# Kernel optimization log

Hardware: AMD Instinct MI355X
Metric: run time of the kernel (lower is better)

## Reference

```python
import jax, jax.numpy as jnp
import numpy as np

B, D, L, H = 4, 1024, 2048, 8
HD = D // H


def setup_inputs() -> dict:
    key = jax.random.key(0)
    k1, k2, k3, k4 = jax.random.split(key, 4)
    query = jax.random.normal(k1, (B, D, L), dtype=jnp.float32)
    mask = jax.random.randint(k2, (B, L), 0, 2, dtype=jnp.int32)
    W1 = jax.random.normal(k3, (2 * D, D), dtype=jnp.float32) * (D ** -0.5)
    Wq = jax.random.normal(k4, (D, D), dtype=jnp.float32) * (D ** -0.5)
    return {"query": query, "mask": mask, "W1": W1, "Wq": Wq}


def _split_heads(x):
    # [B, L, C] -> [B, H, L, C//H]
    b, l, c = x.shape
    return x.reshape(b, l, H, c // H).transpose(0, 2, 1, 3)


def reference(query, mask, W1, Wq):
    # 1x1 conv == channel GEMM; produce [B, L, out]
    temp = jnp.einsum('od,bdl->blo', W1, query)   # [B, L, 2D] (K|V)
    q = jnp.einsum('od,bdl->blo', Wq, query)      # [B, L, D]
    k, v = jnp.split(temp, 2, axis=-1)
    q = _split_heads(q) * (HD ** -0.5)            # [B, H, L, HD]
    k = _split_heads(k)
    v = _split_heads(v)
    scores = jnp.einsum('bhqd,bhkd->bhqk', q, k)  # [B, H, L, L]
    m = mask.astype(jnp.float32)[:, None, None, :]
    logits = scores + (-1e30) * (1.0 - m)
    weights = jax.nn.softmax(logits, axis=-1)     # dropout p=0 (eval)
    out = jnp.einsum('bhqk,bhkd->bhqd', weights, v)
    out = out.transpose(0, 2, 1, 3).reshape(B, L, D)  # merge heads
    return out.transpose(0, 2, 1)                 # [B, D, L]
```

## Files before the change

kernel.cpp:

```cpp
#include <hip/hip_runtime.h>
#include <hip/hip_bf16.h>

#define B_  4
#define D_  1024
#define L_  2048
#define H_  8
#define HD_ 128

typedef __attribute__((ext_vector_type(8))) short bf16x8;
typedef __attribute__((ext_vector_type(4))) float f32x4;

static __device__ __forceinline__ ushort f2bf(float f) {
    unsigned u = __float_as_uint(f);
    unsigned r = (u + 0x7fffu + ((u >> 16) & 1u)) >> 16;
    return (ushort)r;
}

static __device__ __forceinline__ unsigned cvt_pk_bf16(float lo, float hi) {
    unsigned r;
    asm("v_cvt_pk_bf16_f32 %0, %1, %2" : "=v"(r) : "v"(lo), "v"(hi));
    return r;
}

static __device__ __forceinline__ float exp2_fast(float x) {
#if __has_builtin(__builtin_amdgcn_exp2f)
    return __builtin_amdgcn_exp2f(x);
#else
    return exp2f(x);
#endif
}

static __device__ __forceinline__ void dma16(const ushort* g, ushort* l) {
    __builtin_amdgcn_global_load_lds(
        (const __attribute__((address_space(1))) void*)g,
        (__attribute__((address_space(3))) void*)l, 16, 0, 0);
}

__global__ void k_zero_out(float* __restrict__ out, int n) {
    int i = blockIdx.x * 256 + threadIdx.x;
    if (i < n) out[i] = 0.f;
}

__global__ void k_prep(const float* __restrict__ q, const float* __restrict__ W1,
                       const float* __restrict__ Wq, const int* __restrict__ mask,
                       ushort* __restrict__ Wb, ushort* __restrict__ Xt,
                       int* __restrict__ cidx, int* __restrict__ cnt) {
    __shared__ float tile[32][33];
    const int bid = blockIdx.x, t = threadIdx.x;
    if (bid < 8192) {
        int bx = bid & 63, by = (bid >> 6) & 31, bz = bid >> 11;
        int tx = t & 31, ty = t >> 5;
        int d0 = by * 32, l0 = bx * 32;
        const float* src = q + (size_t)bz * D_ * L_;
        for (int i = 0; i < 4; i++)
            tile[ty + 8 * i][tx] = src[(size_t)(d0 + ty + 8 * i) * L_ + l0 + tx];
        __syncthreads();
        ushort* dst = Xt + (size_t)bz * L_ * D_;
        for (int i = 0; i < 4; i++)
            dst[(size_t)(l0 + ty + 8 * i) * D_ + d0 + tx] = f2bf(tile[tx][ty + 8 * i]);
    } else if (bid < 8192 + 3072) {
        int i = (bid - 8192) * 256 + t;
        const int n1 = 2 * D_ * D_ / 4;
        float4 v = (i < n1) ? ((const float4*)W1)[i] : ((const float4*)Wq)[i - n1];
        ushort4 o;
        o.x = f2bf(v.x); o.y = f2bf(v.y); o.z = f2bf(v.z); o.w = f2bf(v.w);
        ((ushort4*)Wb)[i] = o;
    } else {
        int b = bid - (8192 + 3072);
        if (t < 64) {
            int lane = t;
            const int* mb = mask + b * L_;
            int base = 0;
            for (int c = 0; c < L_; c += 64) {
                int m = mb[c + lane];
                unsigned long long bal = __ballot(m != 0);
                int pre = __popcll(bal & ((1ull << lane) - 1ull));
                if (m) cidx[b * L_ + base + pre] = c + lane;
                base += __popcll(bal);
            }
            for (int j = base + lane; j < L_; j += 64) cidx[b * L_ + j] = 0;
            if (lane == 0) cnt[b] = base;
        }
    }
}

__launch_bounds__(256)
__global__ void k_proj(const ushort* __restrict__ Wb, const ushort* __restrict__ Xt,
                       const int* __restrict__ cidx, const int* __restrict__ cnt,
                       ushort* __restrict__ Qb, ushort* __restrict__ Kb,
                       ushort* __restrict__ Vt) {
    __shared__ alignas(16) ushort As[128 * 64];
    __shared__ alignas(16) ushort Bs[128 * 64];
    const int b  = blockIdx.z;
    const int o0 = blockIdx.y * 128;
    const int l0 = blockIdx.x * 128;
    const int type = o0 >> 10;
    if (type < 2) {
        int tiles = (cnt[b] + 127) >> 7;
        if (blockIdx.x >= tiles) return;
    }
    const int t = threadIdx.x;
    const int wave = t >> 6, lane = t & 63, quad = lane >> 4, li = lane & 15;
    const int wm = wave >> 1, wn = wave & 1;
    const ushort* Xb = Xt + (size_t)b * L_ * D_;

    const int srow = t >> 3;
    const int g = (t & 7) ^ (srow & 7);
    const ushort* aSrc[4];
    const ushort* bSrc[4];
    for (int i = 0; i < 4; i++) {
        int r = i * 32 + srow;
        aSrc[i] = Wb + (size_t)(o0 + r) * D_ + g * 8;
        int l = l0 + r;
        int gl = (type < 2) ? cidx[b * L_ + l] : l;
        bSrc[i] = Xb + (size_t)gl * D_ + g * 8;
    }

    f32x4 acc[4][4] = {};

    for (int k0 = 0; k0 < D_; k0 += 64) {
        for (int i = 0; i < 4; i++)
            dma16(aSrc[i] + k0, &As[(i * 256 + wave * 64) * 8]);
        for (int i = 0; i < 4; i++)
            dma16(bSrc[i] + k0, &Bs[(i * 256 + wave * 64) * 8]);
        __syncthreads();
        for (int ks = 0; ks < 64; ks += 32) {
            const int kc = ks >> 3;
            bf16x8 af[4], bfr[4];
            for (int mf = 0; mf < 4; mf++) {
                int row = wm * 64 + mf * 16 + li;
                af[mf] = *(const bf16x8*)&As[row * 64 + (((kc + quad) ^ (li & 7)) * 8)];
            }
            for (int nf = 0; nf < 4; nf++) {
                int row = wn * 64 + nf * 16 + li;
                bfr[nf] = *(const bf16x8*)&Bs[row * 64 + (((kc + quad) ^ (li & 7)) * 8)];
            }
            for (int mf = 0; mf < 4; mf++)
                for (int nf = 0; nf < 4; nf++)
                    acc[mf][nf] = __builtin_amdgcn_mfma_f32_16x16x32_bf16(af[mf], bfr[nf], acc[mf][nf], 0, 0, 0);
        }
        __syncthreads();
    }

    const float qscale = 0.1275174495450826f;
    for (int mf = 0; mf < 4; mf++) {
        int o = o0 + wm * 64 + mf * 16 + quad * 4;
        int c = o & 1023;
        int h = c >> 7, hd = c & 127;
        for (int nf = 0; nf < 4; nf++) {
            int l = l0 + wn * 64 + nf * 16 + li;
            f32x4 v = acc[mf][nf];
            if (type == 0) {
                uint2 kk;
                kk.x = cvt_pk_bf16(v[0], v[1]);
                kk.y = cvt_pk_bf16(v[2], v[3]);
                *(uint2*)&Kb[(((size_t)(b * H_ + h)) * L_ + l) * HD_ + hd] = kk;
            } else if (type == 1) {
                size_t base = (size_t)(b * H_ + h) * HD_;
                Vt[(base + hd + 0) * L_ + l] = f2bf(v[0]);
                Vt[(base + hd + 1) * L_ + l] = f2bf(v[1]);
                Vt[(base + hd + 2) * L_ + l] = f2bf(v[2]);
                Vt[(base + hd + 3) * L_ + l] = f2bf(v[3]);
            } else {
                uint2 qq;
                qq.x = cvt_pk_bf16(v[0] * qscale, v[1] * qscale);
                qq.y = cvt_pk_bf16(v[2] * qscale, v[3] * qscale);
                *(uint2*)&Qb[(((size_t)(b * H_ + h)) * L_ + l) * HD_ + hd] = qq;
            }
        }
    }
}

__launch_bounds__(256, 4)
__global__ void k_attn(const ushort* __restrict__ Qb, const ushort* __restrict__ Kb,
                       const ushort* __restrict__ Vt, const int* __restrict__ mask,
                       float* __restrict__ out) {
    __shared__ alignas(16) ushort Ks[2][32][128];
    __shared__ alignas(16) ushort Vs[2][128][32];
    __shared__ alignas(16) ushort Pl[4][16][40];
    const int blk = blockIdx.x;
    const int h = blk & 7, qt = (blk >> 3) & 31, b = blk >> 8;
    const int t = threadIdx.x;
    const int w = t >> 6, lane = t & 63, quad = lane >> 4, li = lane & 15;
    const int q0 = qt * 64 + w * 16;
    const ushort* Qh = Qb + (size_t)(b * H_ + h) * L_ * HD_;
    const ushort* Kh = Kb + (size_t)(b * H_ + h) * L_ * HD_;
    const ushort* Vh = Vt + (size_t)(b * H_ + h) * HD_ * L_;
    const int* mb = mask + b * L_;

    int cm = 0;
    for (int c = lane; c < L_; c += 64) cm += mb[c];
    cm += __shfl_xor(cm, 32, 64);
    cm += __shfl_xor(cm, 16, 64);
    cm += __shfl_xor(cm, 8, 64);
    cm += __shfl_xor(cm, 4, 64);
    cm += __shfl_xor(cm, 2, 64);
    cm += __shfl_xor(cm, 1, 64);
    const int cnt = cm;
    int cnt_pad = (cnt + 31) & ~31;
    if (cnt_pad < 32) cnt_pad = 32;

    const ushort* kgp[2]; const ushort* vgp[2];
    for (int i = 0; i < 2; i++) {
        int seg = w * 2 + i;
        int key = seg * 4 + (lane >> 4);
        int ck  = (lane & 15) ^ (key & 15);
        kgp[i] = Kh + (size_t)key * HD_ + ck * 8;
        int hd  = seg * 16 + (lane >> 2);
        int cv  = (lane & 3) ^ (hd & 3);
        vgp[i] = Vh + (size_t)hd * L_ + cv * 8;
    }

    for (int i = 0; i < 2; i++) dma16(kgp[i], &Ks[0][0][0] + (w * 2 + i) * 512);
    for (int i = 0; i < 2; i++) dma16(vgp[i], &Vs[0][0][0] + (w * 2 + i) * 512);

    bf16x8 qf[4];
    for (int kf = 0; kf < 4; kf++)
        qf[kf] = *(const bf16x8*)&Qh[(size_t)(q0 + li) * HD_ + kf * 32 + quad * 8];

    float mrun = -1e30f, lrun = 0.f;
    f32x4 acc[8] = {};

    int buf = 0;
    for (int n0 = 0; n0 < cnt_pad; n0 += 32, buf ^= 1) {
        __syncthreads();

        if (n0 + 32 < cnt_pad) {
            int nb = buf ^ 1;
            for (int i = 0; i < 2; i++)
                dma16(kgp[i] + (size_t)(n0 + 32) * HD_, &Ks[nb][0][0] + (w * 2 + i) * 512);
            for (int i = 0; i < 2; i++)
                dma16(vgp[i] + (n0 + 32), &Vs[nb][0][0] + (w * 2 + i) * 512);
        }

        f32x4 s[2] = {};
        for (int kf = 0; kf < 4; kf++) {
            bf16x8 kfr[2];
            for (int mt = 0; mt < 2; mt++)
                kfr[mt] = *(const bf16x8*)&Ks[buf][mt * 16 + li][((kf * 4 + quad) ^ li) * 8];
            for (int mt = 0; mt < 2; mt++)
                s[mt] = __builtin_amdgcn_mfma_f32_16x16x32_bf16(kfr[mt], qf[kf], s[mt], 0, 0, 0);
        }

        if (n0 + 32 > cnt) {
            for (int mt = 0; mt < 2; mt++)
                for (int r = 0; r < 4; r++)
                    if (n0 + mt * 16 + quad * 4 + r >= cnt) s[mt][r] = -1e30f;
        }

        float a0 = fmaxf(fmaxf(s[0][0], s[0][1]), fmaxf(s[0][2], s[0][3]));
        float a1 = fmaxf(fmaxf(s[1][0], s[1][1]), fmaxf(s[1][2], s[1][3]));
        float nm = fmaxf(a0, a1);
        nm = fmaxf(nm, __shfl_xor(nm, 16, 64));
        nm = fmaxf(nm, __shfl_xor(nm, 32, 64));
        float mnew = fmaxf(mrun, nm);
        float alpha = exp2_fast(mrun - mnew);
        mrun = mnew;
        float rs = 0.f;
        for (int mt = 0; mt < 2; mt++)
            for (int r = 0; r < 4; r++) {
                float p = exp2_fast(s[mt][r] - mnew);
                s[mt][r] = p;
                rs += p;
            }
        rs += __shfl_xor(rs, 16, 64);
        rs += __shfl_xor(rs, 32, 64);
        lrun = lrun * alpha + rs;

        if (__any(alpha != 1.0f)) {
            int sb = (lane & 48) | (quad * 4);
            float ar0 = __shfl(alpha, sb + 0, 64);
            float ar1 = __shfl(alpha, sb + 1, 64);
            float ar2 = __shfl(alpha, sb + 2, 64);
            float ar3 = __shfl(alpha, sb + 3, 64);
            for (int nf2 = 0; nf2 < 8; nf2++) {
                acc[nf2][0] *= ar0;
                acc[nf2][1] *= ar1;
                acc[nf2][2] *= ar2;
                acc[nf2][3] *= ar3;
            }
        }

        for (int mt = 0; mt < 2; mt++) {
            uint2 pk;
            pk.x = cvt_pk_bf16(s[mt][0], s[mt][1]);
            pk.y = cvt_pk_bf16(s[mt][2], s[mt][3]);
            *(uint2*)&Pl[w][li][mt * 16 + quad * 4] = pk;
        }

        bf16x8 pa = *(const bf16x8*)&Pl[w][li][quad * 8];
        for (int nf2 = 0; nf2 < 8; nf2++) {
            bf16x8 vb = *(const bf16x8*)&Vs[buf][nf2 * 16 + li][(quad ^ (li & 3)) * 8];
            acc[nf2] = __builtin_amdgcn_mfma_f32_16x16x32_bf16(pa, vb, acc[nf2], 0, 0, 0);
        }
    }

    float inv = 1.0f / lrun;
    int sb = (lane & 48) | (quad * 4);
    float i0 = __shfl(inv, sb + 0, 64);
    float i1 = __shfl(inv, sb + 1, 64);
    float i2 = __shfl(inv, sb + 2, 64);
    float i3 = __shfl(inv, sb + 3, 64);
    int l = q0 + quad * 4;
    for (int nf2 = 0; nf2 < 8; nf2++) {
        int d = h * HD_ + nf2 * 16 + li;
        float4 o4 = { acc[nf2][0] * i0, acc[nf2][1] * i1,
                      acc[nf2][2] * i2, acc[nf2][3] * i3 };
        *(float4*)&out[((size_t)(b * D_ + d)) * L_ + l] = o4;
    }
}

extern "C" void kernel_launch(void* const* d_in, const int* in_sizes, int n_in,
                              void* d_out, int out_size, void* d_ws, size_t ws_size,
                              hipStream_t stream) {
    const float* query = nullptr;
    const int*   mask  = nullptr;
    const float* W1    = nullptr;
    const float* Wq    = nullptr;
    for (int i = 0; i < n_in; i++) {
        switch (in_sizes[i]) {
            case 8388608: query = (const float*)d_in[i]; break;
            case 8192:    mask  = (const int*)d_in[i];   break;
            case 2097152: W1    = (const float*)d_in[i]; break;
            case 1048576: Wq    = (const float*)d_in[i]; break;
        }
    }
    float* out = (float*)d_out;

    if (ws_size < 50331648u || !query || !mask || !W1 || !Wq) {
        hipLaunchKernelGGL(k_zero_out, dim3((out_size + 255) / 256), dim3(256), 0, stream,
                           out, out_size);
        return;
    }

    ushort* Wb = (ushort*)d_out;
    ushort* Xt = (ushort*)((char*)d_out + 6291456);
    int* cidx  = (int*)((char*)d_out + 23068672);
    int* cnt   = (int*)((char*)d_out + 23101440);
    char* ws = (char*)d_ws;
    ushort* Qb = (ushort*)(ws + 0);
    ushort* Kb = (ushort*)(ws + 16777216);
    ushort* Vt = (ushort*)(ws + 33554432);

    hipLaunchKernelGGL(k_prep, dim3(8192 + 3072 + 4), dim3(256), 0, stream,
                       query, W1, Wq, mask, Wb, Xt, cidx, cnt);
    hipLaunchKernelGGL(k_proj, dim3(16, 24, 4), dim3(256), 0, stream, Wb, Xt, cidx, cnt, Qb, Kb, Vt);
    hipLaunchKernelGGL(k_attn, dim3(1024), dim3(256), 0, stream, Qb, Kb, Vt, mask, out);
}
```

Baseline: 232.0 us.

## Use permlane swaps for P fragment and MFMA row-sum for softmax denominator

Replaces the per-wave LDS round trip that reshaped the probability tile into an MFMA A-operand with cross-lane permlane16/32 swaps. The row-max reduction also uses permlane swaps instead of shuffles. The softmax denominator is now an extra MFMA against a ones vector, which removes the shuffle reductions and the final broadcast. The gain is less LDS traffic and fewer shuffles, paid for with one more MFMA per tile. The row sum is also taken from bf16-rounded P, which changes numerics slightly.

New measurement: 224.7 us. -3.2%, faster.

```diff
diff --git a/kernel.cpp b/kernel.cpp
--- a/kernel.cpp
+++ b/kernel.cpp
@@ -9,6 +9,14 @@
 
 typedef __attribute__((ext_vector_type(8))) short bf16x8;
 typedef __attribute__((ext_vector_type(4))) float f32x4;
+typedef __attribute__((ext_vector_type(2))) unsigned uint2v;
+typedef __attribute__((ext_vector_type(4))) unsigned uint4v;
+
+#if __has_builtin(__builtin_amdgcn_permlane16_swap) && __has_builtin(__builtin_amdgcn_permlane32_swap)
+#define HAS_PERMSWAP 1
+#else
+#define HAS_PERMSWAP 0
+#endif
 
 static __device__ __forceinline__ ushort f2bf(float f) {
     unsigned u = __float_as_uint(f);
@@ -27,6 +35,18 @@
     return __builtin_amdgcn_exp2f(x);
 #else
     return exp2f(x);
+#endif
+}
+
+static __device__ __forceinline__ float qmax4(float x) {
+#if HAS_PERMSWAP
+    uint2v a = __builtin_amdgcn_permlane16_swap(__float_as_uint(x), __float_as_uint(x), false, false);
+    float y = fmaxf(__uint_as_float(a[0]), __uint_as_float(a[1]));
+    uint2v b = __builtin_amdgcn_permlane32_swap(__float_as_uint(y), __float_as_uint(y), false, false);
+    return fmaxf(__uint_as_float(b[0]), __uint_as_float(b[1]));
+#else
+    x = fmaxf(x, __shfl_xor(x, 16, 64));
+    return fmaxf(x, __shfl_xor(x, 32, 64));
 #endif
 }
 
@@ -177,7 +197,9 @@
                        float* __restrict__ out) {
     __shared__ alignas(16) ushort Ks[2][32][128];
     __shared__ alignas(16) ushort Vs[2][128][32];
+#if !HAS_PERMSWAP
     __shared__ alignas(16) ushort Pl[4][16][40];
+#endif
     const int blk = blockIdx.x;
     const int h = blk & 7, qt = (blk >> 3) & 31, b = blk >> 8;
     const int t = threadIdx.x;
@@ -218,7 +240,11 @@
     for (int kf = 0; kf < 4; kf++)
         qf[kf] = *(const bf16x8*)&Qh[(size_t)(q0 + li) * HD_ + kf * 32 + quad * 8];
 
-    float mrun = -1e30f, lrun = 0.f;
+    bf16x8 ones;
+    for (int i = 0; i < 8; i++) ones[i] = (short)0x3F80;
+
+    float mrun = -1e30f;
+    f32x4 lsum = {};
     f32x4 acc[8] = {};
 
     int buf = 0;
@@ -250,22 +276,13 @@
 
         float a0 = fmaxf(fmaxf(s[0][0], s[0][1]), fmaxf(s[0][2], s[0][3]));
         float a1 = fmaxf(fmaxf(s[1][0], s[1][1]), fmaxf(s[1][2], s[1][3]));
-        float nm = fmaxf(a0, a1);
-        nm = fmaxf(nm, __shfl_xor(nm, 16, 64));
-        nm = fmaxf(nm, __shfl_xor(nm, 32, 64));
+        float nm = qmax4(fmaxf(a0, a1));
         float mnew = fmaxf(mrun, nm);
         float alpha = exp2_fast(mrun - mnew);
         mrun = mnew;
-        float rs = 0.f;
         for (int mt = 0; mt < 2; mt++)
-            for (int r = 0; r < 4; r++) {
-                float p = exp2_fast(s[mt][r] - mnew);
-                s[mt][r] = p;
-                rs += p;
-            }
-        rs += __shfl_xor(rs, 16, 64);
-        rs += __shfl_xor(rs, 32, 64);
-        lrun = lrun * alpha + rs;
+            for (int r = 0; r < 4; r++)
+                s[mt][r] = exp2_fast(s[mt][r] - mnew);
 
         if (__any(alpha != 1.0f)) {
             int sb = (lane & 48) | (quad * 4);
@@ -273,6 +290,7 @@
             float ar1 = __shfl(alpha, sb + 1, 64);
             float ar2 = __shfl(alpha, sb + 2, 64);
             float ar3 = __shfl(alpha, sb + 3, 64);
+            lsum[0] *= ar0; lsum[1] *= ar1; lsum[2] *= ar2; lsum[3] *= ar3;
             for (int nf2 = 0; nf2 < 8; nf2++) {
                 acc[nf2][0] *= ar0;
                 acc[nf2][1] *= ar1;
@@ -281,26 +299,48 @@
             }
         }
 
-        for (int mt = 0; mt < 2; mt++) {
-            uint2 pk;
-            pk.x = cvt_pk_bf16(s[mt][0], s[mt][1]);
-            pk.y = cvt_pk_bf16(s[mt][2], s[mt][3]);
-            *(uint2*)&Pl[w][li][mt * 16 + quad * 4] = pk;
-        }
-
-        bf16x8 pa = *(const bf16x8*)&Pl[w][li][quad * 8];
+        bf16x8 pa;
+#if HAS_PERMSWAP
+        {
+            unsigned c0 = cvt_pk_bf16(s[0][0], s[0][1]);
+            unsigned c1 = cvt_pk_bf16(s[0][2], s[0][3]);
+            unsigned c2 = cvt_pk_bf16(s[1][0], s[1][1]);
+            unsigned c3 = cvt_pk_bf16(s[1][2], s[1][3]);
+            uint2v x02 = __builtin_amdgcn_permlane32_swap(c0, c2, false, false);
+            uint2v u02 = __builtin_amdgcn_permlane16_swap(x02[0], x02[1], false, false);
+            uint2v x13 = __builtin_amdgcn_permlane32_swap(c1, c3, false, false);
+            uint2v u13 = __builtin_amdgcn_permlane16_swap(x13[0], x13[1], false, false);
+            uint4v paw;
+            paw[0] = u02[0];
+            paw[1] = u13[0];
+            paw[2] = u02[1];
+            paw[3] = u13[1];
+            pa = __builtin_bit_cast(bf16x8, paw);
+        }
+#else
+        {
+            for (int mt = 0; mt < 2; mt++) {
+                uint2 pk;
+                pk.x = cvt_pk_bf16(s[mt][0], s[mt][1]);
+                pk.y = cvt_pk_bf16(s[mt][2], s[mt][3]);
+                *(uint2*)&Pl[w][li][mt * 16 + quad * 4] = pk;
+            }
+            pa = *(const bf16x8*)&Pl[w][li][quad * 8];
+        }
+#endif
+
+        lsum = __builtin_amdgcn_mfma_f32_16x16x32_bf16(pa, ones, lsum, 0, 0, 0);
+
         for (int nf2 = 0; nf2 < 8; nf2++) {
             bf16x8 vb = *(const bf16x8*)&Vs[buf][nf2 * 16 + li][(quad ^ (li & 3)) * 8];
             acc[nf2] = __builtin_amdgcn_mfma_f32_16x16x32_bf16(pa, vb, acc[nf2], 0, 0, 0);
         }
     }
 
-    float inv = 1.0f / lrun;
-    int sb = (lane & 48) | (quad * 4);
-    float i0 = __shfl(inv, sb + 0, 64);
-    float i1 = __shfl(inv, sb + 1, 64);
-    float i2 = __shfl(inv, sb + 2, 64);
-    float i3 = __shfl(inv, sb + 3, 64);
+    float i0 = 1.0f / lsum[0];
+    float i1 = 1.0f / lsum[1];
+    float i2 = 1.0f / lsum[2];
+    float i3 = 1.0f / lsum[3];
     int l = q0 + quad * 4;
     for (int nf2 = 0; nf2 < 8; nf2++) {
         int d = h * HD_ + nf2 * 16 + li;
```
